# Performance work log

Hardware: AMD Instinct MI355X
Metric: run time of the kernel (lower is better)

Reference implementation:

```python
import jax, jax.numpy as jnp
import numpy as np

B, L, D, DF, E, R = 4, 1024, 1024, 4096, 32768, 64
EPS = 1e-6


def layer_norm(x, g, b, eps=EPS):
    mu = x.mean(-1, keepdims=True)
    var = ((x - mu) ** 2).mean(-1, keepdims=True)
    return (x - mu) * jax.lax.rsqrt(var + eps) * g + b


def setup_inputs() -> dict:
    key = jax.random.key(0)
    ks = jax.random.split(key, 16)
    s = 0.02
    return {
        "hidden_states": jax.random.normal(ks[0], (B, L, D), jnp.float32),
        "rel_table": jax.random.normal(ks[1], (R, D), jnp.float32) * s,
        "Wq": jax.random.normal(ks[2], (D, D), jnp.float32) * s,
        "bq": jnp.zeros((D,), jnp.float32),
        "Wk": jax.random.normal(ks[3], (D, D), jnp.float32) * s,
        "Wv": jax.random.normal(ks[4], (D, D), jnp.float32) * s,
        "Wo": jax.random.normal(ks[5], (D, D), jnp.float32) * s,
        "bo": jnp.zeros((D,), jnp.float32),
        "ln0_g": jnp.ones((D,), jnp.float32),
        "ln0_b": jnp.zeros((D,), jnp.float32),
        "ln1_g": jnp.ones((D,), jnp.float32),
        "ln1_b": jnp.zeros((D,), jnp.float32),
        "W1": jax.random.normal(ks[6], (D, DF), jnp.float32) * s,
        "b1": jnp.zeros((DF,), jnp.float32),
        "W2": jax.random.normal(ks[7], (DF, D), jnp.float32) * s,
        "b2": jnp.zeros((D,), jnp.float32),
        "ln2_g": jnp.ones((D,), jnp.float32),
        "ln2_b": jnp.zeros((D,), jnp.float32),
        "edge_src": jax.random.randint(ks[8], (B, E), 0, L, jnp.int32),
        "edge_dst": jax.random.randint(ks[9], (B, E), 0, L, jnp.int32),
        "edge_rel": jax.random.randint(ks[10], (B, E), 0, R, jnp.int32),
    }


def reference(hidden_states, rel_table, Wq, bq, Wk, Wv, Wo, bo,
              ln0_g, ln0_b, ln1_g, ln1_b, W1, b1, W2, b2, ln2_g, ln2_b,
              edge_src, edge_dst, edge_rel):
    scale = np.sqrt(D).astype(np.float32)  # num_heads=1 -> d_k = D
    hs_norm = layer_norm(hidden_states, ln0_g, ln0_b)

    def rgat_one(x, src, dst, rel):
        # x: [L, D]; src/dst/rel: [E]
        e = rel_table[rel]                       # [E, D] relation embeddings
        q = x @ Wq + bq
        k = x @ Wk
        v = x @ Wv
        score = jnp.sum((k[src] + e) * q[dst], axis=-1) / scale      # [E]
        score = jnp.exp(jnp.clip(score, -10.0, 10.0))
        wv = jax.ops.segment_sum((v[src] + e) * score[:, None], dst, num_segments=L)
        z = jax.ops.segment_sum(score, dst, num_segments=L)          # [L]
        o = wv / z[:, None]
        out = layer_norm(x + o @ Wo + bo, ln1_g, ln1_b)
        ffn = jnp.maximum(out @ W1 + b1, 0.0) @ W2 + b2
        return layer_norm(out + ffn, ln2_g, ln2_b)

    graph_rep = jax.vmap(rgat_one)(hs_norm, edge_src, edge_dst, edge_rel)
    out = jax.nn.elu(graph_rep)                  # dropout = identity (eval)
    return hidden_states + out
```

## Files before the change

### kernel.cpp

```cpp
#include <hip/hip_runtime.h>
#include <hip/hip_bf16.h>

#define B_SZ 4
#define L_SEQ 1024
#define D_MODEL 1024
#define DF_FF 4096
#define E_PER_B 32768
#define R_REL 64
#define M_ROWS (B_SZ * L_SEQ)

typedef __attribute__((ext_vector_type(8))) short bf16x8;
typedef __attribute__((ext_vector_type(4))) float f32x4;

__device__ inline float b2f(unsigned short u) {
    union { unsigned int i; float f; } x; x.i = ((unsigned int)u) << 16; return x.f;
}
__device__ inline unsigned short f2b(float f) {
    union { float f; unsigned int u; } x; x.f = f;
    unsigned int r = x.u + 0x7FFFu + ((x.u >> 16) & 1u);
    return (unsigned short)(r >> 16);
}

#define GLOBAL_CAST(p) ((const __attribute__((address_space(1))) void*)(p))
#define LDS_CAST(p)    ((__attribute__((address_space(3))) void*)(p))

#define BT_QKV (1024u * 3072u)
#define SEXT_M 1152
#define LDA_WV 1088
#define LDB_WVP 1152
#define BT_WVP (1024u * 1152u)

__global__ void prep_all(const float* __restrict__ Wq, const float* __restrict__ Wk,
                         const float* __restrict__ Wv, const float* __restrict__ Wo,
                         const float* __restrict__ W1, const float* __restrict__ W2,
                         const float* __restrict__ rel, const float* __restrict__ bq,
                         const float* __restrict__ hidden,
                         const float* __restrict__ ln0_g, const float* __restrict__ ln0_b,
                         unsigned short* __restrict__ Wqkv_t, unsigned short* __restrict__ Wo_t,
                         unsigned short* __restrict__ W1_t, unsigned short* __restrict__ W2_t,
                         unsigned short* __restrict__ relbPad,
                         float* __restrict__ bqkv,
                         unsigned short* __restrict__ Xn_b16,
                         float* __restrict__ zeroReg) {
    __shared__ float tile[32][33];
    __shared__ float sb1[4], sb2[4];
    const int id = blockIdx.x, tid = threadIdx.x;
    if (id < 12288) {
        const float* src; unsigned short* dst; int K, N, x, y;
        if (id < 4096) {
            const int seg = id >> 10, t = id & 1023;
            K = 1024; N = 1024; x = t & 31; y = t >> 5;
            src = (seg == 0) ? Wq : (seg == 1) ? Wk : (seg == 2) ? Wv : Wo;
            dst = (seg == 3) ? Wo_t : (Wqkv_t + (size_t)seg * 1048576);
        } else if (id < 8192) {
            const int t = id - 4096; K = 1024; N = 4096; x = t & 127; y = t >> 7;
            src = W1; dst = W1_t;
        } else {
            const int t = id - 8192; K = 4096; N = 1024; x = t & 31; y = t >> 5;
            src = W2; dst = W2_t;
        }
        const int n0 = x * 32, k0 = y * 32, tx = tid & 31, ty = tid >> 5;
#pragma unroll
        for (int r = 0; r < 32; r += 8)
            tile[ty + r][tx] = src[(size_t)(k0 + ty + r) * N + (n0 + tx)];
        __syncthreads();
#pragma unroll
        for (int r = 0; r < 32; r += 8)
            dst[(size_t)(n0 + ty + r) * K + (k0 + tx)] = f2b(tile[tx][ty + r]);
    } else if (id < 12800) {
        const int i = (id - 12288) * 256 + tid;
        relbPad[i] = (i < 65536) ? f2b(rel[i]) : (unsigned short)0;
    } else if (id < 12812) {
        const int i = (id - 12800) * 256 + tid;
        bqkv[i] = (i < 1024) ? bq[i] : 0.0f;
    } else if (id < 16908) {
        const int row = id - 12812, t = tid;
        const size_t base = (size_t)row * 1024 + t * 4;
        float4 xv = *(const float4*)(hidden + base);
        float x0 = xv.x, x1 = xv.y, x2 = xv.z, x3 = xv.w;
        float s = x0 + x1 + x2 + x3;
#pragma unroll
        for (int o = 32; o > 0; o >>= 1) s += __shfl_down(s, o);
        if ((t & 63) == 0) sb1[t >> 6] = s;
        __syncthreads();
        const float mu = (sb1[0] + sb1[1] + sb1[2] + sb1[3]) * (1.0f / 1024.0f);
        const float d0 = x0 - mu, d1 = x1 - mu, d2 = x2 - mu, d3 = x3 - mu;
        float s2 = d0 * d0 + d1 * d1 + d2 * d2 + d3 * d3;
#pragma unroll
        for (int o = 32; o > 0; o >>= 1) s2 += __shfl_down(s2, o);
        if ((t & 63) == 0) sb2[t >> 6] = s2;
        __syncthreads();
        const float var = (sb2[0] + sb2[1] + sb2[2] + sb2[3]) * (1.0f / 1024.0f);
        const float rstd = rsqrtf(var + 1e-6f);
        const float4 gv = *(const float4*)(ln0_g + t * 4);
        const float4 bv = *(const float4*)(ln0_b + t * 4);
        ushort4 ob;
        ob.x = f2b(d0 * rstd * gv.x + bv.x);
        ob.y = f2b(d1 * rstd * gv.y + bv.y);
        ob.z = f2b(d2 * rstd * gv.z + bv.z);
        ob.w = f2b(d3 * rstd * gv.w + bv.w);
        *(ushort4*)(Xn_b16 + base) = ob;
    } else {
        const size_t base = (size_t)(id - 16908) * 4096 + tid * 4;
        const float4 z4 = make_float4(0.f, 0.f, 0.f, 0.f);
#pragma unroll
        for (int j = 0; j < 4; j++)
            *(float4*)(zeroReg + base + j * 1024) = z4;
    }
}

__device__ inline void tile_swizzle(int id, int ntn, int& tm, int& tn) {
    tm = ((id & 7) + ((id >> 3) / ntn) * 8) * 128;
    tn = ((id >> 3) % ntn) * 128;
}
__device__ inline void tsw256(int id, int ntn, int& tm, int& tn) {
    tm = ((id & 7) + ((id >> 3) / ntn) * 8) * 256;
    tn = ((id >> 3) % ntn) * 256;
}

#define GEMM_BODY(GA, LDA_, GB, LDB_, KLEN)                                                 \
    f32x4 acc[4][4];                                                                        \
    _Pragma("unroll") for (int i = 0; i < 4; i++)                                           \
        _Pragma("unroll") for (int j = 0; j < 4; j++) acc[i][j] = (f32x4)0.0f;              \
    for (int k0 = 0; k0 < (KLEN); k0 += 64) {                                               \
        __syncthreads();                                                                    \
        _Pragma("unroll") for (int r = 0; r < 4; ++r) {                                     \
            __builtin_amdgcn_global_load_lds(GLOBAL_CAST((GA) + (size_t)r * 8 * (LDA_)),    \
                LDS_CAST(&lA[(wave * 32 + r * 8) * 64]), 16, 0, 0);                         \
            __builtin_amdgcn_global_load_lds(GLOBAL_CAST((GB) + (size_t)r * 8 * (LDB_)),    \
                LDS_CAST(&lB[(wave * 32 + r * 8) * 64]), 16, 0, 0);                         \
        }                                                                                   \
        (GA) += 64; (GB) += 64;                                                             \
        __builtin_amdgcn_s_waitcnt(0);                                                      \
        __syncthreads();                                                                    \
        _Pragma("unroll") for (int kk = 0; kk < 2; ++kk) {                                  \
            const int cb = kk * 4 + quad;                                                   \
            bf16x8 af[4], bf[4];                                                            \
            _Pragma("unroll") for (int i = 0; i < 4; i++) {                                 \
                const int ra = wm + i * 16 + l16;                                           \
                af[i] = *(const bf16x8*)&lA[ra * 64 + ((cb ^ (ra & 7)) * 8)];               \
                const int rb = wn + i * 16 + l16;                                           \
                bf[i] = *(const bf16x8*)&lB[rb * 64 + ((cb ^ (rb & 7)) * 8)];               \
            }                                                                               \
            _Pragma("unroll") for (int mi = 0; mi < 4; mi++)                                \
                _Pragma("unroll") for (int ni = 0; ni < 4; ni++)                            \
                    acc[mi][ni] = __builtin_amdgcn_mfma_f32_16x16x32_bf16(                  \
                        af[mi], bf[ni], acc[mi][ni], 0, 0, 0);                              \
        }                                                                                   \
    }

#define ST_A2(bufc, hh, kt) { \
    _Pragma("unroll") for (int j = 0; j < 2; j++) \
        __builtin_amdgcn_global_load_lds(GLOBAL_CAST(gA[hh][j] + (size_t)(kt) * 64), \
            LDS_CAST(&ls[bufc][0][((hh) * 128 + j * 64 + wv * 8) * 64]), 16, 0, 0); }
#define ST_B2(bufc, hh, kt) { \
    _Pragma("unroll") for (int j = 0; j < 2; j++) \
        __builtin_amdgcn_global_load_lds(GLOBAL_CAST(gB[hh][j] + (size_t)(kt) * 64), \
            LDS_CAST(&ls[bufc][1][((hh) * 128 + j * 64 + wv * 8) * 64]), 16, 0, 0); }

#define VM2 asm volatile("s_waitcnt vmcnt(2)" ::: "memory")
#define VM0 asm volatile("s_waitcnt vmcnt(0)" ::: "memory")

#define PHASE(bufc, hhw, kkc, RB, STMT, WAITSTMT) { \
    STMT; \
    const int slotx = ((((kkc) * 4) + quad) ^ (l16 & 7)) * 8; \
    if (RB) { \
        _Pragma("unroll") for (int ni = 0; ni < 4; ni++) \
            pbf[ni] = *(const bf16x8*)&ls[bufc][1][(wc * 64 + ni * 16 + l16) * 64 + slotx]; \
    } \
    bf16x8 paf[4]; \
    _Pragma("unroll") for (int m4 = 0; m4 < 4; m4++) \
        paf[m4] = *(const bf16x8*)&ls[bufc][0][(wm * 128 + (hhw) * 64 + m4 * 16 + l16) * 64 + slotx]; \
    asm volatile("s_waitcnt lgkmcnt(0)" ::: "memory"); \
    __builtin_amdgcn_sched_barrier(0); \
    __builtin_amdgcn_s_setprio(1); \
    _Pragma("unroll") for (int m4 = 0; m4 < 4; m4++) \
        _Pragma("unroll") for (int ni = 0; ni < 4; ni++) \
            acc[(hhw) * 4 + m4][ni] = __builtin_amdgcn_mfma_f32_16x16x32_bf16( \
                paf[m4], pbf[ni], acc[(hhw) * 4 + m4][ni], 0, 0, 0); \
    __builtin_amdgcn_s_setprio(0); \
    WAITSTMT; \
    __builtin_amdgcn_s_barrier(); }

template<bool RELU, bool SPLITK>
__global__ __launch_bounds__(512, 2)
void gemm256(const unsigned short* __restrict__ A, int lda,
             const unsigned short* __restrict__ Bt, int ldb,
             const float* __restrict__ bias,
             unsigned short* __restrict__ C, size_t pstride,
             int N, int Kc, int ntn) {
    __shared__ unsigned short ls[2][2][16384];
    int tile_m, tile_n;
    tsw256(blockIdx.x, ntn, tile_m, tile_n);
    const int t = threadIdx.x;
    const int wv = t >> 6, lane = t & 63;
    const int wm = wv >> 2;
    const int wc = wv & 3;
    const int quad = lane >> 4, l16 = lane & 15;
    const int srow8 = lane >> 3;
    const int schunk = ((lane & 7) ^ srow8) * 8;
    const int z = SPLITK ? blockIdx.z : 0;
    const int kofs = z * Kc;

    const unsigned short* gA[2][2];
    const unsigned short* gB[2][2];
#pragma unroll
    for (int h = 0; h < 2; h++)
#pragma unroll
        for (int j = 0; j < 2; j++) {
            gA[h][j] = A + (size_t)(tile_m + h * 128 + j * 64 + wv * 8 + srow8) * lda + kofs + schunk;
            gB[h][j] = Bt + (size_t)(tile_n + h * 128 + j * 64 + wv * 8 + srow8) * ldb + kofs + schunk;
        }

    f32x4 acc[8][4];
#pragma unroll
    for (int i = 0; i < 8; i++)
#pragma unroll
        for (int j = 0; j < 4; j++) acc[i][j] = (f32x4)0.0f;
    bf16x8 pbf[4];

    ST_A2(0, 0, 0); ST_A2(0, 1, 0); ST_B2(0, 0, 0); ST_B2(0, 1, 0);
    ST_B2(1, 0, 1);
    VM2;
    __builtin_amdgcn_s_barrier();

    const int NI = Kc >> 7;
    for (int it = 0; it < NI - 1; ++it) {
        const int ks = 2 * it;
        PHASE(0, 0, 0, 1, ST_A2(1, 0, ks + 1), )
        PHASE(0, 1, 0, 0, ST_A2(1, 1, ks + 1), )
        PHASE(0, 0, 1, 1, ST_B2(1, 1, ks + 1), )
        PHASE(0, 1, 1, 0, ST_B2(0, 0, ks + 2), VM2)
        PHASE(1, 0, 0, 1, ST_A2(0, 0, ks + 2), )
        PHASE(1, 1, 0, 0, ST_A2(0, 1, ks + 2), )
        PHASE(1, 0, 1, 1, ST_B2(0, 1, ks + 2), )
        PHASE(1, 1, 1, 0, ST_B2(1, 0, ks + 3), VM2)
    }
    {
        const int ks = 2 * (NI - 1);
        PHASE(0, 0, 0, 1, ST_A2(1, 0, ks + 1), )
        PHASE(0, 1, 0, 0, ST_A2(1, 1, ks + 1), )
        PHASE(0, 0, 1, 1, ST_B2(1, 1, ks + 1), )
        PHASE(0, 1, 1, 0, , VM0)
        PHASE(1, 0, 0, 1, , )
        PHASE(1, 1, 0, 0, , )
        PHASE(1, 0, 1, 1, , )
        PHASE(1, 1, 1, 0, , )
    }

    unsigned short* Co = C + (SPLITK ? (size_t)z * pstride : 0);
#pragma unroll
    for (int mi = 0; mi < 8; mi++) {
#pragma unroll
        for (int ni = 0; ni < 4; ni++) {
            const int col = tile_n + wc * 64 + ni * 16 + l16;
            const float bv = (SPLITK && z != 0) ? 0.0f : bias[col];
#pragma unroll
            for (int r = 0; r < 4; r++) {
                const int row = tile_m + wm * 128 + mi * 16 + quad * 4 + r;
                float v = acc[mi][ni][r] + bv;
                if (RELU) v = fmaxf(v, 0.0f);
                Co[(size_t)row * N + col] = f2b(v);
            }
        }
    }
}

__global__ __launch_bounds__(256, 4)
void sext_w(const unsigned short* __restrict__ QKV,
            const unsigned short* __restrict__ relPad,
            const unsigned short* __restrict__ Wo_t,
            unsigned short* __restrict__ Pbase,
            unsigned short* __restrict__ Bwvp, int Kc) {
    __shared__ unsigned short lA[128 * 64];
    __shared__ unsigned short lB[128 * 64];
    const int id = blockIdx.x, t = threadIdx.x;
    const int wave = t >> 6, lane = t & 63;
    const int wm = (wave >> 1) * 64, wn = (wave & 1) * 64;
    const int quad = lane >> 4, l16 = lane & 15;
    const int srow = lane >> 3;
    const int schunk = ((lane & 7) ^ srow) * 8;

    if (id >= 576) {
        const int t2 = id - 576;
        const int b = t2 / 72, rem = t2 % 72;
        const int tile_m = (rem / 9) * 128;
        const int tile_n = (rem % 9) * 128;
        const unsigned short* gA = Wo_t + (size_t)(tile_m + wave * 32 + srow) * 1024 + schunk;
        const int brow = tile_n + wave * 32 + srow;
        const unsigned short* gB;
        size_t ldb;
        if (tile_n < 1024) {
            gB = QKV + (size_t)b * BT_QKV + (size_t)brow * 3072 + 2048 + schunk;
            ldb = 3072;
        } else {
            gB = relPad + (size_t)(brow - 1024) * 1024 + schunk;
            ldb = 1024;
        }
        GEMM_BODY(gA, 1024, gB, ldb, 1024)
        unsigned short* P = Bwvp + (size_t)b * BT_WVP;
#pragma unroll
        for (int mi = 0; mi < 4; mi++) {
#pragma unroll
            for (int ni = 0; ni < 4; ni++) {
                const int col = tile_n + wn + ni * 16 + l16;
#pragma unroll
                for (int r = 0; r < 4; r++) {
                    const int row = tile_m + wm + mi * 16 + quad * 4 + r;
                    P[(size_t)row * LDB_WVP + col] = f2b(acc[mi][ni][r]);
                }
            }
        }
        return;
    }

    const int bx = id % 72, b = (id / 72) & 3, z = id / 288;
    const int tile_m = (bx >> 3) * 128;
    const int tile_n = (bx & 7) * 128;
    const int kofs = z * Kc;
    const int arow = tile_m + wave * 32 + srow;
    const unsigned short* gA;
    size_t lda;
    if (tile_m < 1024) {
        gA = QKV + (size_t)b * BT_QKV + (size_t)arow * 3072 + 1024 + kofs + schunk;
        lda = 3072;
    } else {
        gA = relPad + (size_t)(arow - 1024) * 1024 + kofs + schunk;
        lda = 1024;
    }
    const unsigned short* gB = QKV + (size_t)b * BT_QKV
                                   + (size_t)(tile_n + wave * 32 + srow) * 3072 + kofs + schunk;
    GEMM_BODY(gA, lda, gB, 3072, Kc)
    unsigned short* P = Pbase + ((size_t)z * B_SZ + b) * (SEXT_M * 1024);
#pragma unroll
    for (int mi = 0; mi < 4; mi++) {
#pragma unroll
        for (int ni = 0; ni < 4; ni++) {
            const int col = tile_n + wn + ni * 16 + l16;
#pragma unroll
            for (int r = 0; r < 4; r++) {
                const int row = tile_m + wm + mi * 16 + quad * 4 + r;
                P[(size_t)row * 1024 + col] = f2b(acc[mi][ni][r]);
            }
        }
    }
}

__global__ __launch_bounds__(256, 4)
void gemm_wv_splitk(const unsigned short* __restrict__ A,
                    const unsigned short* __restrict__ Bt,
                    const float* __restrict__ bias,
                    unsigned short* __restrict__ Pbase, size_t pstride) {
    __shared__ unsigned short lA[128 * 64];
    __shared__ unsigned short lB[128 * 64];
    int tile_m, tile_n;
    tile_swizzle(blockIdx.x, 8, tile_m, tile_n);
    const int z = blockIdx.z;
    const int kofs = z * 576;
    const int Kc = z ? 512 : 576;
    const int t = threadIdx.x;
    const int wave = t >> 6, lane = t & 63;
    const int wm = (wave >> 1) * 64, wn = (wave & 1) * 64;
    const int quad = lane >> 4, l16 = lane & 15;
    const int srow = lane >> 3;
    const int schunk = ((lane & 7) ^ srow) * 8;
    const unsigned short* gA = A + (size_t)(tile_m + wave * 32 + srow) * LDA_WV + kofs + schunk;
    const unsigned short* gB = Bt + (size_t)(tile_m >> 10) * BT_WVP
                                  + (size_t)(tile_n + wave * 32 + srow) * LDB_WVP + kofs + schunk;
    GEMM_BODY(gA, LDA_WV, gB, LDB_WVP, Kc)
    unsigned short* P = Pbase + (size_t)z * pstride;
#pragma unroll
    for (int mi = 0; mi < 4; mi++) {
#pragma unroll
        for (int ni = 0; ni < 4; ni++) {
            const int col = tile_n + wn + ni * 16 + l16;
            const float bv = (z == 0) ? bias[col] : 0.0f;
#pragma unroll
            for (int r = 0; r < 4; r++) {
                const int row = tile_m + wm + mi * 16 + quad * 4 + r;
                P[(size_t)row * 1024 + col] = f2b(acc[mi][ni][r] + bv);
            }
        }
    }
}

template<bool FINAL, int NR>
__global__ void ln_kernel(const unsigned short* __restrict__ Xb,
                          const unsigned short* __restrict__ Rbase, size_t rstride,
                          const float* __restrict__ g, const float* __restrict__ be,
                          unsigned short* __restrict__ ob16,
                          const float* __restrict__ hidden, float* __restrict__ fout) {
    __shared__ float sb1[4], sb2[4];
    const int row = blockIdx.x, t = threadIdx.x;
    const size_t base = (size_t)row * 1024 + t * 4;

    ushort4 xv = *(const ushort4*)(Xb + base);
    float x0 = b2f(xv.x), x1 = b2f(xv.y), x2 = b2f(xv.z), x3 = b2f(xv.w);
#pragma unroll
    for (int r = 0; r < NR; r++) {
        ushort4 rv = *(const ushort4*)(Rbase + r * rstride + base);
        x0 += b2f(rv.x); x1 += b2f(rv.y); x2 += b2f(rv.z); x3 += b2f(rv.w);
    }
    float s = x0 + x1 + x2 + x3;
#pragma unroll
    for (int o = 32; o > 0; o >>= 1) s += __shfl_down(s, o);
    if ((t & 63) == 0) sb1[t >> 6] = s;
    __syncthreads();
    const float mu = (sb1[0] + sb1[1] + sb1[2] + sb1[3]) * (1.0f / 1024.0f);

    const float d0 = x0 - mu, d1 = x1 - mu, d2 = x2 - mu, d3 = x3 - mu;
    float s2 = d0 * d0 + d1 * d1 + d2 * d2 + d3 * d3;
#pragma unroll
    for (int o = 32; o > 0; o >>= 1) s2 += __shfl_down(s2, o);
    if ((t & 63) == 0) sb2[t >> 6] = s2;
    __syncthreads();
    const float var = (sb2[0] + sb2[1] + sb2[2] + sb2[3]) * (1.0f / 1024.0f);
    const float rstd = rsqrtf(var + 1e-6f);

    const float4 gv = *(const float4*)(g + t * 4);
    const float4 bv = *(const float4*)(be + t * 4);
    const float y0 = d0 * rstd * gv.x + bv.x;
    const float y1 = d1 * rstd * gv.y + bv.y;
    const float y2 = d2 * rstd * gv.z + bv.z;
    const float y3 = d3 * rstd * gv.w + bv.w;

    if (!FINAL) {
        ushort4 ob; ob.x = f2b(y0); ob.y = f2b(y1); ob.z = f2b(y2); ob.w = f2b(y3);
        *(ushort4*)(ob16 + base) = ob;
    } else {
        const float4 hv = *(const float4*)(hidden + base);
        const float e0 = y0 > 0.0f ? y0 : expm1f(y0);
        const float e1 = y1 > 0.0f ? y1 : expm1f(y1);
        const float e2 = y2 > 0.0f ? y2 : expm1f(y2);
        const float e3 = y3 > 0.0f ? y3 : expm1f(y3);
        float4 o; o.x = hv.x + e0; o.y = hv.y + e1; o.z = hv.z + e2; o.w = hv.w + e3;
        *(float4*)(fout + base) = o;
    }
}

__global__ void edge_scatter(const unsigned short* __restrict__ S,
                             const int* __restrict__ src, const int* __restrict__ dst,
                             const int* __restrict__ rel,
                             float* __restrict__ A, float* __restrict__ G) {
    const size_t ZSTR = (size_t)B_SZ * SEXT_M * 1024;
    const int gg = blockIdx.x * 256 + threadIdx.x;
    const int b = gg >> 15;
    const int s = src[gg], d = dst[gg], r = rel[gg];
    const size_t sbase = ((size_t)b * SEXT_M + s) * 1024 + d;
    const size_t tbase = ((size_t)b * SEXT_M + 1024 + r) * 1024 + d;
    const float sval = b2f(S[sbase]) + b2f(S[sbase + ZSTR]);
    const float tval = b2f(S[tbase]) + b2f(S[tbase + ZSTR]);
    float sc = (sval + tval) * (1.0f / 32.0f);
    sc = expf(fminf(fmaxf(sc, -10.0f), 10.0f));
    atomicAdd(&A[((size_t)((b << 10) + d) << 10) + s], sc);
    atomicAdd(&G[((size_t)((b << 10) + d) << 6) + r], sc);
}

__global__ void normalize(const float* __restrict__ A, const float* __restrict__ G,
                          unsigned short* __restrict__ Awv) {
    __shared__ float sInv;
    const int row = blockIdx.x, t = threadIdx.x;
    float v = 0.0f;
    if (t < 64) {
        v = G[(size_t)row * 64 + t];
        float s = v;
#pragma unroll
        for (int o = 1; o < 64; o <<= 1) s += __shfl_xor(s, o);
        if (t == 0) sInv = 1.0f / s;
    }
    __syncthreads();
    const float inv = sInv;
    const size_t obase = (size_t)row * LDA_WV;
    const float4 a = *(const float4*)(A + (size_t)row * 1024 + t * 4);
    ushort4 o;
    o.x = f2b(a.x * inv); o.y = f2b(a.y * inv); o.z = f2b(a.z * inv); o.w = f2b(a.w * inv);
    *(ushort4*)(Awv + obase + t * 4) = o;
    if (t < 16) {
        const float4 gq = *(const float4*)(G + (size_t)row * 64 + t * 4);
        ushort4 og;
        og.x = f2b(gq.x * inv); og.y = f2b(gq.y * inv);
        og.z = f2b(gq.z * inv); og.w = f2b(gq.w * inv);
        *(ushort4*)(Awv + obase + 1024 + t * 4) = og;
    }
}

extern "C" void kernel_launch(void* const* d_in, const int* in_sizes, int n_in,
                              void* d_out, int out_size, void* d_ws, size_t ws_size,
                              hipStream_t stream) {
    const float* hidden  = (const float*)d_in[0];
    const float* rel_tbl = (const float*)d_in[1];
    const float* Wq = (const float*)d_in[2];
    const float* bq = (const float*)d_in[3];
    const float* Wk = (const float*)d_in[4];
    const float* Wv = (const float*)d_in[5];
    const float* Wo = (const float*)d_in[6];
    const float* bo = (const float*)d_in[7];
    const float* ln0_g = (const float*)d_in[8];
    const float* ln0_b = (const float*)d_in[9];
    const float* ln1_g = (const float*)d_in[10];
    const float* ln1_b = (const float*)d_in[11];
    const float* W1 = (const float*)d_in[12];
    const float* b1 = (const float*)d_in[13];
    const float* W2 = (const float*)d_in[14];
    const float* b2 = (const float*)d_in[15];
    const float* ln2_g = (const float*)d_in[16];
    const float* ln2_b = (const float*)d_in[17];
    const int* esrc = (const int*)d_in[18];
    const int* edst = (const int*)d_in[19];
    const int* erel = (const int*)d_in[20];
    float* out = (float*)d_out;

    char* ws = (char*)d_ws;
    const size_t MB = 1024 * 1024;
    unsigned short* Xn_b16  = (unsigned short*)(ws + 16 * MB);
    unsigned short* H1      = (unsigned short*)(ws + 0);
    unsigned short* Wqkv_t  = (unsigned short*)(ws + 24 * MB);
    unsigned short* Wo_t    = (unsigned short*)(ws + 30 * MB);
    unsigned short* W1_t    = (unsigned short*)(ws + 32 * MB);
    unsigned short* W2_t    = (unsigned short*)(ws + 40 * MB);
    unsigned short* relbPad = (unsigned short*)(ws + 48 * MB);
    float*          bqkv    = (float*)(ws + 48 * MB + 512 * 1024);
    unsigned short* QKV     = (unsigned short*)(ws + 49 * MB);
    unsigned short* Awv     = (unsigned short*)(ws + 49 * MB);
    unsigned short* Qw2H    = (unsigned short*)(ws + 49 * MB);
    unsigned short* PwoH    = (unsigned short*)(ws + 66 * MB);
    unsigned short* SxH     = (unsigned short*)(ws + 73 * MB);
    unsigned short* Bwvp    = (unsigned short*)(ws + 92 * MB);
    float*          Amat    = (float*)(ws + 101 * MB);
    float*          Gmat    = (float*)(ws + 117 * MB);
    unsigned short* Out_b16 = (unsigned short*)(ws + 113 * MB);

    const size_t PSTRIDE_H = 4u * 1024 * 1024;
    const dim3 blk(256);
    const dim3 blk512(512);

    prep_all<<<17996, blk, 0, stream>>>(Wq, Wk, Wv, Wo, W1, W2, rel_tbl, bq,
                                        hidden, ln0_g, ln0_b,
                                        Wqkv_t, Wo_t, W1_t, W2_t, relbPad, bqkv,
                                        Xn_b16, Amat);
    gemm256<false, false><<<dim3(192), blk512, 0, stream>>>(
        Xn_b16, 1024, Wqkv_t, 1024, bqkv, QKV, 0, 3072, 1024, 12);
    sext_w<<<864, blk, 0, stream>>>(QKV, relbPad, Wo_t, SxH, Bwvp, 512);
    edge_scatter<<<512, blk, 0, stream>>>(SxH, esrc, edst, erel, Amat, Gmat);
    normalize<<<M_ROWS, blk, 0, stream>>>(Amat, Gmat, Awv);
    gemm_wv_splitk<<<dim3(256, 1, 2), blk, 0, stream>>>(Awv, Bwvp, bo, PwoH, PSTRIDE_H);
    ln_kernel<false, 2><<<M_ROWS, blk, 0, stream>>>(Xn_b16, PwoH, PSTRIDE_H, ln1_g, ln1_b,
                                                    Out_b16, nullptr, nullptr);
    gemm256<true, false><<<dim3(256), blk512, 0, stream>>>(
        Out_b16, 1024, W1_t, 1024, b1, H1, 0, 4096, 1024, 16);
    gemm256<false, true><<<dim3(64, 1, 4), blk512, 0, stream>>>(
        H1, 4096, W2_t, 4096, b2, Qw2H, PSTRIDE_H, 1024, 1024, 4);
    ln_kernel<true, 4><<<M_ROWS, blk, 0, stream>>>(Out_b16, Qw2H, PSTRIDE_H, ln2_g, ln2_b,
                                                   nullptr, hidden, out);
    (void)in_sizes; (void)n_in; (void)out_size; (void)ws_size;
}
```

Baseline: 351.4 us.

## Restructure 256-tile GEMM main loop into quadrant ping-pong with register prefetch

Reorganizes the gemm256 inner loop so each phase computes one quadrant of the output using both k-halves, with A and B fragments double-buffered in registers (a0f/a1f, b0f/b1f). LDS reads for the next phase are issued before the MFMAs of the current phase, waiting only on partial lgkmcnt. Global-to-LDS staging is split into quarter-tile loads interleaved across phases. The aim is to hide LDS read latency behind MFMA work, at the cost of more registers and a fragile hand-tuned wait-count schedule.

```diff
diff --git a/kernel.cpp b/kernel.cpp
--- a/kernel.cpp
+++ b/kernel.cpp
@@ -149,37 +149,45 @@
         }                                                                                   \
     }
 
-#define ST_A2(bufc, hh, kt) { \
-    _Pragma("unroll") for (int j = 0; j < 2; j++) \
-        __builtin_amdgcn_global_load_lds(GLOBAL_CAST(gA[hh][j] + (size_t)(kt) * 64), \
-            LDS_CAST(&ls[bufc][0][((hh) * 128 + j * 64 + wv * 8) * 64]), 16, 0, 0); }
-#define ST_B2(bufc, hh, kt) { \
-    _Pragma("unroll") for (int j = 0; j < 2; j++) \
-        __builtin_amdgcn_global_load_lds(GLOBAL_CAST(gB[hh][j] + (size_t)(kt) * 64), \
-            LDS_CAST(&ls[bufc][1][((hh) * 128 + j * 64 + wv * 8) * 64]), 16, 0, 0); }
-
-#define VM2 asm volatile("s_waitcnt vmcnt(2)" ::: "memory")
-#define VM0 asm volatile("s_waitcnt vmcnt(0)" ::: "memory")
-
-#define PHASE(bufc, hhw, kkc, RB, STMT, WAITSTMT) { \
-    STMT; \
-    const int slotx = ((((kkc) * 4) + quad) ^ (l16 & 7)) * 8; \
-    if (RB) { \
-        _Pragma("unroll") for (int ni = 0; ni < 4; ni++) \
-            pbf[ni] = *(const bf16x8*)&ls[bufc][1][(wc * 64 + ni * 16 + l16) * 64 + slotx]; \
-    } \
-    bf16x8 paf[4]; \
-    _Pragma("unroll") for (int m4 = 0; m4 < 4; m4++) \
-        paf[m4] = *(const bf16x8*)&ls[bufc][0][(wm * 128 + (hhw) * 64 + m4 * 16 + l16) * 64 + slotx]; \
-    asm volatile("s_waitcnt lgkmcnt(0)" ::: "memory"); \
+#define ST_Aq(bufc, QM, kt) { \
+    _Pragma("unroll") for (int j_ = 0; j_ < 2; j_++) { \
+        const int u_ = j_ * 8 + wv; \
+        const int lr_ = ((u_ >> 3) * 128) + (QM) * 64 + ((u_ & 7) * 8); \
+        __builtin_amdgcn_global_load_lds(GLOBAL_CAST(Ag + (size_t)lr_ * lda + (kt) * 64), \
+            LDS_CAST(&ls[bufc][0][lr_ * 64]), 16, 0, 0); } }
+#define ST_Bq(bufc, QN, kt) { \
+    _Pragma("unroll") for (int j_ = 0; j_ < 2; j_++) { \
+        const int u_ = j_ * 8 + wv; \
+        const int lr_ = ((u_ >> 2) * 64) + (QN) * 32 + ((u_ & 3) * 8); \
+        __builtin_amdgcn_global_load_lds(GLOBAL_CAST(Bg + (size_t)lr_ * ldb + (kt) * 64), \
+            LDS_CAST(&ls[bufc][1][lr_ * 64]), 16, 0, 0); } }
+
+#define RD_A(SLOT, bufc, QM) { \
+    _Pragma("unroll") for (int m4_ = 0; m4_ < 4; m4_++) \
+        _Pragma("unroll") for (int kk_ = 0; kk_ < 2; kk_++) \
+            SLOT[m4_][kk_] = *(const bf16x8*)&ls[bufc][0][ \
+                (wm * 128 + (QM) * 64 + m4_ * 16 + l16) * 64 + (((kk_ * 4 + quad) ^ (l16 & 7)) * 8)]; }
+#define RD_B(SLOT, bufc, QN) { \
+    _Pragma("unroll") for (int n2_ = 0; n2_ < 2; n2_++) \
+        _Pragma("unroll") for (int kk_ = 0; kk_ < 2; kk_++) \
+            SLOT[n2_][kk_] = *(const bf16x8*)&ls[bufc][1][ \
+                (wc * 64 + (QN) * 32 + n2_ * 16 + l16) * 64 + (((kk_ * 4 + quad) ^ (l16 & 7)) * 8)]; }
+
+#define VM4 asm volatile("s_waitcnt vmcnt(4)" ::: "memory");
+#define VM0 asm volatile("s_waitcnt vmcnt(0)" ::: "memory");
+
+#define PHX(STAGES, READS, LG, ASLOT, BSLOT, QM, QN, VMW) { \
+    STAGES; READS; \
+    asm volatile("s_waitcnt lgkmcnt(" #LG ")" ::: "memory"); \
     __builtin_amdgcn_sched_barrier(0); \
     __builtin_amdgcn_s_setprio(1); \
-    _Pragma("unroll") for (int m4 = 0; m4 < 4; m4++) \
-        _Pragma("unroll") for (int ni = 0; ni < 4; ni++) \
-            acc[(hhw) * 4 + m4][ni] = __builtin_amdgcn_mfma_f32_16x16x32_bf16( \
-                paf[m4], pbf[ni], acc[(hhw) * 4 + m4][ni], 0, 0, 0); \
+    _Pragma("unroll") for (int m4_ = 0; m4_ < 4; m4_++) \
+        _Pragma("unroll") for (int n2_ = 0; n2_ < 2; n2_++) \
+            _Pragma("unroll") for (int kk_ = 0; kk_ < 2; kk_++) \
+                acc[(QM) * 4 + m4_][(QN) * 2 + n2_] = __builtin_amdgcn_mfma_f32_16x16x32_bf16( \
+                    ASLOT[m4_][kk_], BSLOT[n2_][kk_], acc[(QM) * 4 + m4_][(QN) * 2 + n2_], 0, 0, 0); \
     __builtin_amdgcn_s_setprio(0); \
-    WAITSTMT; \
+    VMW; \
     __builtin_amdgcn_s_barrier(); }
 
 template<bool RELU, bool SPLITK>
@@ -202,50 +210,44 @@
     const int z = SPLITK ? blockIdx.z : 0;
     const int kofs = z * Kc;
 
-    const unsigned short* gA[2][2];
-    const unsigned short* gB[2][2];
-#pragma unroll
-    for (int h = 0; h < 2; h++)
-#pragma unroll
-        for (int j = 0; j < 2; j++) {
-            gA[h][j] = A + (size_t)(tile_m + h * 128 + j * 64 + wv * 8 + srow8) * lda + kofs + schunk;
-            gB[h][j] = Bt + (size_t)(tile_n + h * 128 + j * 64 + wv * 8 + srow8) * ldb + kofs + schunk;
-        }
+    const unsigned short* Ag = A + (size_t)(tile_m + srow8) * lda + kofs + schunk;
+    const unsigned short* Bg = Bt + (size_t)(tile_n + srow8) * ldb + kofs + schunk;
 
     f32x4 acc[8][4];
 #pragma unroll
     for (int i = 0; i < 8; i++)
 #pragma unroll
         for (int j = 0; j < 4; j++) acc[i][j] = (f32x4)0.0f;
-    bf16x8 pbf[4];
-
-    ST_A2(0, 0, 0); ST_A2(0, 1, 0); ST_B2(0, 0, 0); ST_B2(0, 1, 0);
-    ST_B2(1, 0, 1);
-    VM2;
+    bf16x8 a0f[4][2], a1f[4][2], b0f[2][2], b1f[2][2];
+
+    ST_Aq(0, 0, 0) ST_Aq(0, 1, 0) ST_Bq(0, 0, 0) ST_Bq(0, 1, 0)
+    ST_Aq(1, 0, 1) ST_Bq(1, 1, 1) ST_Aq(1, 1, 1)
+    asm volatile("s_waitcnt vmcnt(6)" ::: "memory");
     __builtin_amdgcn_s_barrier();
+    RD_A(a0f, 0, 0) RD_B(b0f, 0, 0)
 
     const int NI = Kc >> 7;
     for (int it = 0; it < NI - 1; ++it) {
-        const int ks = 2 * it;
-        PHASE(0, 0, 0, 1, ST_A2(1, 0, ks + 1), )
-        PHASE(0, 1, 0, 0, ST_A2(1, 1, ks + 1), )
-        PHASE(0, 0, 1, 1, ST_B2(1, 1, ks + 1), )
-        PHASE(0, 1, 1, 0, ST_B2(0, 0, ks + 2), VM2)
-        PHASE(1, 0, 0, 1, ST_A2(0, 0, ks + 2), )
-        PHASE(1, 1, 0, 0, ST_A2(0, 1, ks + 2), )
-        PHASE(1, 0, 1, 1, ST_B2(0, 1, ks + 2), )
-        PHASE(1, 1, 1, 0, ST_B2(1, 0, ks + 3), VM2)
+        const int t1 = 2 * it + 1, s0 = 2 * it + 2, s1 = 2 * it + 3;
+        PHX(ST_Bq(1, 0, t1), RD_B(b1f, 0, 1),                   4,  a0f, b0f, 0, 0, )
+        PHX(ST_Aq(0, 0, s0), RD_A(a1f, 0, 1),                   8,  a0f, b1f, 0, 1, )
+        PHX(ST_Bq(0, 1, s0), ,                                  0,  a1f, b1f, 1, 1, VM4)
+        PHX(ST_Aq(0, 1, s0), RD_A(a0f, 1, 0) RD_B(b1f, 1, 0),   12, a1f, b0f, 1, 0, )
+        PHX(ST_Bq(0, 0, s0), RD_B(b0f, 1, 1),                   4,  a0f, b1f, 0, 0, )
+        PHX(ST_Aq(1, 0, s1), RD_A(a1f, 1, 1),                   8,  a0f, b0f, 0, 1, )
+        PHX(ST_Bq(1, 1, s1), ,                                  0,  a1f, b0f, 1, 1, VM4)
+        PHX(ST_Aq(1, 1, s1), RD_A(a0f, 0, 0) RD_B(b0f, 0, 0),   12, a1f, b1f, 1, 0, )
     }
     {
-        const int ks = 2 * (NI - 1);
-        PHASE(0, 0, 0, 1, ST_A2(1, 0, ks + 1), )
-        PHASE(0, 1, 0, 0, ST_A2(1, 1, ks + 1), )
-        PHASE(0, 0, 1, 1, ST_B2(1, 1, ks + 1), )
-        PHASE(0, 1, 1, 0, , VM0)
-        PHASE(1, 0, 0, 1, , )
-        PHASE(1, 1, 0, 0, , )
-        PHASE(1, 0, 1, 1, , )
-        PHASE(1, 1, 1, 0, , )
+        const int t1 = 2 * NI - 1;
+        PHX(ST_Bq(1, 0, t1), RD_B(b1f, 0, 1),                   4,  a0f, b0f, 0, 0, )
+        PHX(,                RD_A(a1f, 0, 1),                   8,  a0f, b1f, 0, 1, )
+        PHX(,                ,                                  0,  a1f, b1f, 1, 1, VM0)
+        PHX(,                RD_A(a0f, 1, 0) RD_B(b1f, 1, 0),   12, a1f, b0f, 1, 0, )
+        PHX(,                RD_B(b0f, 1, 1),                   4,  a0f, b1f, 0, 0, )
+        PHX(,                RD_A(a1f, 1, 1),                   8,  a0f, b0f, 0, 1, )
+        PHX(,                ,                                  0,  a1f, b0f, 1, 1, )
+        PHX(,                ,                                  0,  a1f, b1f, 1, 0, )
     }
 
     unsigned short* Co = C + (SPLITK ? (size_t)z * pstride : 0);
```

Result: slower. 601.8 us (+71.3%).
